# Kernel tuning notes

Measured on AMD Instinct MI355X. Metric: run time of the kernel, lower is better.

Reference implementation:

```python
import jax, jax.numpy as jnp
import numpy as np

B, S, A, H, Z = 256, 512, 64, 1024, 256

def setup_inputs() -> dict:
    key = jax.random.key(0)
    ks = jax.random.split(key, 24)
    w = lambda k, shape: (jax.random.normal(k, shape, jnp.float32) * 0.02)
    inp = {
        "x": jax.random.randint(ks[0], (B, S), 0, A),
        "h0": jax.random.normal(ks[1], (B, H), jnp.float32),            # init_hidden randn
        "eps": jax.random.normal(ks[2], (S + 1, B, Z), jnp.float32),     # reparam noise per step + final
        "phi_x_w": w(ks[3], (H, A)),  "phi_x_b": jnp.zeros((H,), jnp.float32),
        "enc_w1": w(ks[4], (H, 2 * H)), "enc_b1": jnp.zeros((H,), jnp.float32),
        "enc_w2": w(ks[5], (Z, H)),     "enc_b2": jnp.zeros((Z,), jnp.float32),
        "pri_w1": w(ks[6], (H, H)),     "pri_b1": jnp.zeros((H,), jnp.float32),
        "pri_w2": w(ks[7], (Z, H)),     "pri_b2": jnp.zeros((Z,), jnp.float32),
        "phi_z_w": w(ks[8], (H, Z)),    "phi_z_b": jnp.zeros((H,), jnp.float32),
        "dec_w": w(ks[9], (H, 2 * H)),  "dec_b": jnp.zeros((H,), jnp.float32),
        "act_w": w(ks[10], (A, H)),     "act_b": jnp.zeros((A,), jnp.float32),
        "gru_wih": w(ks[11], (3 * H, 2 * H)), "gru_whh": w(ks[12], (3 * H, H)),
        "gru_bih": jnp.zeros((3 * H,), jnp.float32), "gru_bhh": jnp.zeros((3 * H,), jnp.float32),
    }
    return inp

def reference(x, h0, eps, phi_x_w, phi_x_b, enc_w1, enc_b1, enc_w2, enc_b2,
              pri_w1, pri_b1, pri_w2, pri_b2, phi_z_w, phi_z_b, dec_w, dec_b,
              act_w, act_b, gru_wih, gru_whh, gru_bih, gru_bhh):
    relu, sp = jax.nn.relu, jax.nn.softplus

    def gru_cell(xin, h):  # PyTorch GRU gate math
        gi = xin @ gru_wih.T + gru_bih
        gh = h @ gru_whh.T + gru_bhh
        ir, iz, inn = jnp.split(gi, 3, axis=-1)
        hr, hz, hn = jnp.split(gh, 3, axis=-1)
        r = jax.nn.sigmoid(ir + hr)
        zg = jax.nn.sigmoid(iz + hz)
        n = jnp.tanh(inn + r * hn)
        return (1.0 - zg) * n + zg * h

    def prior(h):
        p = relu(h @ pri_w1.T + pri_b1) @ pri_w2.T + pri_b2
        return p, sp(p)

    x_oh = jax.nn.one_hot(x, A, dtype=jnp.float32).transpose(1, 0, 2)  # [S,B,A]

    def step(carry, inp):
        h, kld = carry
        x_t, eps_t = inp
        px = relu(x_t @ phi_x_w.T + phi_x_b)                            # [B,H]
        enc = relu(jnp.concatenate([px, h], -1) @ enc_w1.T + enc_b1) @ enc_w2.T + enc_b2
        enc_std = sp(enc)
        pri_m, pri_std = prior(h)
        kld_el = (2 * jnp.log(pri_std) - 2 * jnp.log(enc_std)
                  + (enc_std ** 2 + (enc - pri_m) ** 2) / pri_std ** 2 - 1.0)
        kld = kld + 0.5 * jnp.sum(kld_el)
        z_t = eps_t * enc_std + enc                                     # reparam sample
        pz = relu(z_t @ phi_z_w.T + phi_z_b)
        h_new = gru_cell(jnp.concatenate([px, pz], -1), h)
        return (h_new, kld), None

    (h, kld), _ = jax.lax.scan(step, (h0, jnp.float32(0.0)), (x_oh, eps[:S]))

    pri_m, pri_std = prior(h)
    z_t = eps[S] * pri_std + pri_m
    pz = relu(z_t @ phi_z_w.T + phi_z_b)
    dec = relu(jnp.concatenate([pz, h], -1) @ dec_w.T + dec_b)
    pred_act = dec @ act_w.T + act_b
    return pred_act, kld
```

## Files before the change

### kernel.cpp

```cpp
#include <hip/hip_runtime.h>


typedef float f32x4 __attribute__((ext_vector_type(4)));
typedef __bf16 bf16x8 __attribute__((ext_vector_type(8)));

#define BB 256
#define SS 512
#define HH 1024
#define ZZ 256
#define AA 64
#define NWG 256

__device__ __forceinline__ float softplus_(float x) {
    return (x > 15.f) ? x : log1pf(expf(x));
}
__device__ __forceinline__ float sigmoid_(float x) {
    return 1.f / (1.f + expf(-x));
}

__device__ __forceinline__ void gbar(unsigned* bar, unsigned p, int wg) {
    __syncthreads();
    if (threadIdx.x == 0) {
        unsigned s = p & 7u;
        unsigned exp = (p >> 3) + 1u;
        unsigned* leaf = bar + (s * 8 + (wg >> 5)) * 16;
        unsigned* root = bar + (64 + s) * 16;
        unsigned* flag = bar + (72 + s) * 16;
        unsigned old = __hip_atomic_fetch_add(leaf, 1u, __ATOMIC_ACQ_REL, __HIP_MEMORY_SCOPE_AGENT);
        if (old == 32u * exp - 1u) {
            unsigned old2 = __hip_atomic_fetch_add(root, 1u, __ATOMIC_ACQ_REL, __HIP_MEMORY_SCOPE_AGENT);
            if (old2 == 8u * exp - 1u) {
                __hip_atomic_store(flag, exp, __ATOMIC_RELEASE, __HIP_MEMORY_SCOPE_AGENT);
            }
        }
        while (__hip_atomic_load(flag, __ATOMIC_ACQUIRE, __HIP_MEMORY_SCOPE_AGENT) < exp) {
            __builtin_amdgcn_s_sleep(2);
        }
    }
    __syncthreads();
}

__device__ __forceinline__ void xbar(unsigned* flags, int g, int rank, int ngrp,
                                     unsigned tok) {
    __syncthreads();
    if (threadIdx.x == 0)
        __hip_atomic_store(flags + g * 256 + rank, tok, __ATOMIC_RELAXED,
                           __HIP_MEMORY_SCOPE_AGENT);
    unsigned l = threadIdx.x & 63;
    unsigned* base = flags + g * 256;
    for (;;) {
        bool ok = true;
        for (int i = (int)l; i < ngrp; i += 64)
            ok &= (__hip_atomic_load(base + i, __ATOMIC_RELAXED,
                                     __HIP_MEMORY_SCOPE_AGENT) >= tok);
        if (__all(ok)) break;
        __builtin_amdgcn_s_sleep(2);
    }
    asm volatile("buffer_inv sc0" ::: "memory");
}

template<int MT, int NT>
__device__ __forceinline__ void wgemm(const __bf16* __restrict__ A, int lda, int mstride,
                                      const __bf16* __restrict__ B, int ldb, int nstride,
                                      int K, f32x4 (&acc)[MT][NT]) {
    int lane = threadIdx.x & 63;
    int rr = lane & 15;
    int ko = (lane >> 4) * 8;
    const __bf16* ap = A + rr * lda + ko;
    const __bf16* bp = B + rr * ldb + ko;
    #pragma unroll 2
    for (int k = 0; k < K; k += 32) {
        bf16x8 af[MT], bfr[NT];
        #pragma unroll
        for (int mt = 0; mt < MT; mt++) af[mt] = *(const bf16x8*)(ap + mt * mstride + k);
        #pragma unroll
        for (int nt = 0; nt < NT; nt++) bfr[nt] = *(const bf16x8*)(bp + nt * nstride + k);
        #pragma unroll
        for (int mt = 0; mt < MT; mt++)
            #pragma unroll
            for (int nt = 0; nt < NT; nt++)
                acc[mt][nt] = __builtin_amdgcn_mfma_f32_16x16x32_bf16(af[mt], bfr[nt], acc[mt][nt], 0, 0, 0);
    }
}


__global__ void k_zeroctl(unsigned* bar, unsigned* flags, unsigned* cnt, float* kldacc) {
    for (int i = threadIdx.x; i < 1280; i += 256) bar[i] = 0u;
    for (int i = threadIdx.x; i < 2048; i += 256) flags[i] = 0u;
    if (threadIdx.x < 8) cnt[threadIdx.x] = 0u;
    if (threadIdx.x == 0) *kldacc = 0.f;
}

__global__ void k_pack(const float* __restrict__ src, int src_ld, int col_off,
                       __bf16* __restrict__ dst, int cols, int total) {
    int i = blockIdx.x * 256 + threadIdx.x;
    if (i >= total) return;
    int r = i / cols, c = i - r * cols;
    dst[i] = (__bf16)src[r * src_ld + col_off + c];
}

__global__ void k_copyf(const float* __restrict__ s, float* __restrict__ d, int n) {
    int i = blockIdx.x * 256 + threadIdx.x;
    if (i < n) d[i] = s[i];
}

__global__ void k_px(const float* __restrict__ phi_x_w, const float* __restrict__ phi_x_b,
                     float* __restrict__ px) {
    int i = blockIdx.x * 256 + threadIdx.x;
    int a = i >> 10, hh = i & 1023;
    px[i] = fmaxf(phi_x_w[hh * AA + a] + phi_x_b[hh], 0.f);
}

__global__ __launch_bounds__(256) void k_tables(const float* __restrict__ enc_w1,
                                                const float* __restrict__ wih,
                                                const float* __restrict__ px,
                                                float* __restrict__ encpx,
                                                float* __restrict__ gipx) {
    __shared__ float spx[64][65];
    int tid = threadIdx.x;
    int cg = blockIdx.x * 4 + (tid >> 6);
    int a = tid & 63;
    const float* wrow = (cg < 1024) ? (enc_w1 + cg * 2048) : (wih + (cg - 1024) * 2048);
    float sum = 0.f;
    for (int k0 = 0; k0 < 1024; k0 += 64) {
        __syncthreads();
        for (int e = tid; e < 4096; e += 256)
            spx[e >> 6][e & 63] = px[((e >> 6) << 10) + k0 + (e & 63)];
        __syncthreads();
        #pragma unroll 8
        for (int kk = 0; kk < 64; kk++) sum += wrow[k0 + kk] * spx[a][kk];
    }
    if (cg < 1024) encpx[a * 1024 + cg] = sum;
    else gipx[a * 3072 + (cg - 1024)] = sum;
}


struct PArgs {
    const int* x; const float* eps;
    const __bf16 *WA, *W2, *WPZ, *WIH, *WHH, *WDEC, *WACT;
    const float *encpx, *gipx;
    const float *eb1, *pb1, *eb2, *pb2, *pzb, *decb, *actb, *bih, *bhh;
    float *hf0, *hf1; __bf16 *hb0, *hb1;
    __bf16 *hidcat, *zbuf, *pzbuf, *tailhid, *decbuf;
    float *gh; float *kldacc; unsigned *bar, *flags, *cnt;
    float* out;
};

__global__ __launch_bounds__(256) void k_persist(PArgs a) {
    int wg = blockIdx.x;
    int tid = threadIdx.x;
    int v = tid >> 6;
    int lane = tid & 63;
    int rr = lane & 15;
    int ko = (lane >> 4) * 8;
    int col = lane & 15, rq = (lane >> 4) * 4;
    float kl = 0.f;
    float* hf[2] = {a.hf0, a.hf1};
    __bf16* hb[2] = {a.hb0, a.hb1};

    __shared__ float lds2[4][2][256];
    __shared__ int sh_g, sh_rank, sh_ngrp;
    __shared__ float sh_kl[4];

    if (tid == 0) {
        unsigned xcc = __builtin_amdgcn_s_getreg((31 << 11) | (0 << 6) | 20) & 7u;
        sh_g = (int)xcc;
        sh_rank = (int)atomicAdd(a.cnt + xcc, 1u);
    }
    __syncthreads();
    int g = sh_g, rank = sh_rank;
    gbar(a.bar, 0, wg);
    if (tid == 0)
        sh_ngrp = (int)__hip_atomic_load(a.cnt + g, __ATOMIC_RELAXED,
                                         __HIP_MEMORY_SCOPE_AGENT);
    __syncthreads();
    int ngrp = sh_ngrp;
    int base_m = g * 32;

    unsigned tok = 1;

    for (int t = 0; t < SS; t++) {
        int cur = t & 1, nxt = cur ^ 1;

        for (int r = rank; r < 32; r += ngrp) {
            int mt = v >> 1;
            int nt0 = r * 10 + (v & 1) * 5;
            const __bf16* ap = hb[cur] + (size_t)(base_m + mt * 16 + rr) * HH + ko;
            const __bf16* bp[5];
            #pragma unroll
            for (int j = 0; j < 5; j++) {
                int n = (nt0 + j) * 16 + rr;
                bp[j] = ((n < 2048) ? (a.WA + (size_t)n * HH)
                                    : (a.WHH + (size_t)(n - 2048) * HH)) + ko;
            }
            f32x4 acc[5] = {};
            #pragma unroll 2
            for (int k = 0; k < HH; k += 32) {
                bf16x8 af = *(const bf16x8*)(ap + k);
                #pragma unroll
                for (int j = 0; j < 5; j++)
                    acc[j] = __builtin_amdgcn_mfma_f32_16x16x32_bf16(
                        af, *(const bf16x8*)(bp[j] + k), acc[j], 0, 0, 0);
            }
            int xb[4];
            #pragma unroll
            for (int i = 0; i < 4; i++)
                xb[i] = a.x[(base_m + mt * 16 + rq + i) * SS + t];
            #pragma unroll
            for (int j = 0; j < 5; j++) {
                int c0 = (nt0 + j) * 16 + col;
                if (c0 < 1024) {
                    float bias = a.eb1[c0];
                    #pragma unroll
                    for (int i = 0; i < 4; i++) {
                        int m = base_m + mt * 16 + rq + i;
                        float val = acc[j][i] + bias + a.encpx[xb[i] * 1024 + c0];
                        a.hidcat[m * 2048 + c0] = (__bf16)fmaxf(val, 0.f);
                    }
                } else if (c0 < 2048) {
                    float bias = a.pb1[c0 - 1024];
                    #pragma unroll
                    for (int i = 0; i < 4; i++) {
                        int m = base_m + mt * 16 + rq + i;
                        a.hidcat[m * 2048 + c0] = (__bf16)fmaxf(acc[j][i] + bias, 0.f);
                    }
                } else {
                    int gc = c0 - 2048;
                    #pragma unroll
                    for (int i = 0; i < 4; i++) {
                        int m = base_m + mt * 16 + rq + i;
                        a.gh[m * 3072 + gc] = acc[j][i];
                    }
                }
            }
        }
        xbar(a.flags, g, rank, ngrp, tok++);

        for (int r = rank; r < 32; r += ngrp) {
            int mtl = r >> 4, zsl = r & 15;
            const __bf16* ae_p = a.hidcat + (size_t)(base_m + mtl * 16 + rr) * 2048 + v * 256 + ko;
            const __bf16* ap_p = ae_p + 1024;
            const __bf16* be_p = a.W2 + (size_t)(zsl * 16 + rr) * HH + v * 256 + ko;
            const __bf16* bp_p = a.W2 + (size_t)(256 + zsl * 16 + rr) * HH + v * 256 + ko;
            f32x4 ae = {0.f,0.f,0.f,0.f}, av = {0.f,0.f,0.f,0.f};
            #pragma unroll
            for (int k = 0; k < 256; k += 32) {
                ae = __builtin_amdgcn_mfma_f32_16x16x32_bf16(
                    *(const bf16x8*)(ae_p + k), *(const bf16x8*)(be_p + k), ae, 0, 0, 0);
                av = __builtin_amdgcn_mfma_f32_16x16x32_bf16(
                    *(const bf16x8*)(ap_p + k), *(const bf16x8*)(bp_p + k), av, 0, 0, 0);
            }
            #pragma unroll
            for (int i = 0; i < 4; i++) {
                int idx = (rq + i) * 16 + col;
                lds2[v][0][idx] = ae[i];
                lds2[v][1][idx] = av[i];
            }
            __syncthreads();
            {
                float e = lds2[0][0][tid] + lds2[1][0][tid] + lds2[2][0][tid] + lds2[3][0][tid];
                float pv = lds2[0][1][tid] + lds2[1][1][tid] + lds2[2][1][tid] + lds2[3][1][tid];
                int m = base_m + mtl * 16 + (tid >> 4);
                int z = zsl * 16 + (tid & 15);
                float enc = e + a.eb2[z];
                float pri = pv + a.pb2[z];
                float es = softplus_(enc), ps = softplus_(pri);
                float d = enc - pri;
                kl += 2.f * (logf(ps) - logf(es)) + (es * es + d * d) / (ps * ps) - 1.f;
                const float* epst = a.eps + (size_t)t * BB * ZZ;
                a.zbuf[m * ZZ + z] = (__bf16)(epst[m * ZZ + z] * es + enc);
            }
            __syncthreads();
        }
        xbar(a.flags, g, rank, ngrp, tok++);

        for (int r = rank; r < 32; r += ngrp) {
            int mt = v >> 1;
            int nt = r * 2 + (v & 1);
            const __bf16* ap = a.zbuf + (size_t)(base_m + mt * 16 + rr) * ZZ + ko;
            const __bf16* bp = a.WPZ + (size_t)(nt * 16 + rr) * ZZ + ko;
            f32x4 acc = {0.f,0.f,0.f,0.f};
            #pragma unroll
            for (int k = 0; k < ZZ; k += 32)
                acc = __builtin_amdgcn_mfma_f32_16x16x32_bf16(
                    *(const bf16x8*)(ap + k), *(const bf16x8*)(bp + k), acc, 0, 0, 0);
            int n = nt * 16 + col;
            float b = a.pzb[n];
            #pragma unroll
            for (int i = 0; i < 4; i++) {
                int m = base_m + mt * 16 + rq + i;
                a.pzbuf[m * HH + n] = (__bf16)fmaxf(acc[i] + b, 0.f);
            }
        }
        xbar(a.flags, g, rank, ngrp, tok++);

        for (int r = rank; r < 32; r += ngrp) {
            int mt = v >> 1;
            int jt = r * 2 + (v & 1);
            const __bf16* ap = a.pzbuf + (size_t)(base_m + mt * 16 + rr) * HH + ko;
            const __bf16* bp0 = a.WIH + (size_t)(jt * 16 + rr) * HH + ko;
            const __bf16* bp1g = bp0 + (size_t)1024 * HH;
            const __bf16* bp2g = bp0 + (size_t)2048 * HH;
            f32x4 acc[3] = {};
            #pragma unroll 2
            for (int k = 0; k < HH; k += 32) {
                bf16x8 af = *(const bf16x8*)(ap + k);
                acc[0] = __builtin_amdgcn_mfma_f32_16x16x32_bf16(af, *(const bf16x8*)(bp0 + k), acc[0], 0, 0, 0);
                acc[1] = __builtin_amdgcn_mfma_f32_16x16x32_bf16(af, *(const bf16x8*)(bp1g + k), acc[1], 0, 0, 0);
                acc[2] = __builtin_amdgcn_mfma_f32_16x16x32_bf16(af, *(const bf16x8*)(bp2g + k), acc[2], 0, 0, 0);
            }
            int j = jt * 16 + col;
            float br = a.bih[j], bz2 = a.bih[1024 + j], bn = a.bih[2048 + j];
            float cr = a.bhh[j], cz = a.bhh[1024 + j], cn = a.bhh[2048 + j];
            #pragma unroll
            for (int i = 0; i < 4; i++) {
                int m = base_m + mt * 16 + rq + i;
                int xb = a.x[m * SS + t];
                const float* gp = a.gipx + xb * 3072;
                float gir = acc[0][i] + gp[j] + br;
                float giz = acc[1][i] + gp[1024 + j] + bz2;
                float gin = acc[2][i] + gp[2048 + j] + bn;
                float ghr = a.gh[m * 3072 + j] + cr;
                float ghz = a.gh[m * 3072 + 1024 + j] + cz;
                float ghn = a.gh[m * 3072 + 2048 + j] + cn;
                float rg = sigmoid_(gir + ghr);
                float zg = sigmoid_(giz + ghz);
                float nn = tanhf(gin + rg * ghn);
                float hv = (1.f - zg) * nn + zg * hf[cur][m * HH + j];
                hf[nxt][m * HH + j] = hv;
                hb[nxt][m * HH + j] = (__bf16)hv;
            }
        }
        xbar(a.flags, g, rank, ngrp, tok++);
    }

    for (int r = rank; r < 32; r += ngrp) {
        int mt = v >> 1, nt = r * 2 + (v & 1);
        f32x4 acc[1][1] = {};
        wgemm<1, 1>(hb[0] + (size_t)(base_m + mt * 16) * HH, HH, 0,
                    a.WA + (size_t)(1024 + nt * 16) * HH, HH, 0, HH, acc);
        int n = nt * 16 + col;
        float b = a.pb1[n];
        #pragma unroll
        for (int i = 0; i < 4; i++) {
            int m = base_m + mt * 16 + rq + i;
            a.tailhid[m * HH + n] = (__bf16)fmaxf(acc[0][0][i] + b, 0.f);
        }
    }
    xbar(a.flags, g, rank, ngrp, tok++);
    if (v == 0) {
        for (int r = rank; r < 32; r += ngrp) {
            int mtl = r >> 4, zt = r & 15;
            f32x4 apv[1][1] = {};
            wgemm<1, 1>(a.tailhid + (size_t)(base_m + mtl * 16) * HH, HH, 0,
                        a.W2 + (size_t)(256 + zt * 16) * HH, HH, 0, HH, apv);
            int z = zt * 16 + col;
            float bp = a.pb2[z];
            const float* epst = a.eps + (size_t)SS * BB * ZZ;
            #pragma unroll
            for (int i = 0; i < 4; i++) {
                int m = base_m + mtl * 16 + rq + i;
                float pri = apv[0][0][i] + bp;
                float ps = softplus_(pri);
                a.zbuf[m * ZZ + z] = (__bf16)(epst[m * ZZ + z] * ps + pri);
            }
        }
    }
    xbar(a.flags, g, rank, ngrp, tok++);
    for (int r = rank; r < 32; r += ngrp) {
        int mt = v >> 1, nt = r * 2 + (v & 1);
        f32x4 acc[1][1] = {};
        wgemm<1, 1>(a.zbuf + (size_t)(base_m + mt * 16) * ZZ, ZZ, 0,
                    a.WPZ + (size_t)(nt * 16) * ZZ, ZZ, 0, ZZ, acc);
        int n = nt * 16 + col;
        float b = a.pzb[n];
        #pragma unroll
        for (int i = 0; i < 4; i++) {
            int m = base_m + mt * 16 + rq + i;
            a.pzbuf[m * HH + n] = (__bf16)fmaxf(acc[0][0][i] + b, 0.f);
        }
    }
    xbar(a.flags, g, rank, ngrp, tok++);
    for (int r = rank; r < 32; r += ngrp) {
        int mt = v >> 1, nt = r * 2 + (v & 1);
        f32x4 acc[1][1] = {};
        wgemm<1, 1>(a.pzbuf + (size_t)(base_m + mt * 16) * HH, HH, 0,
                    a.WDEC + (size_t)(nt * 16) * 2048, 2048, 0, HH, acc);
        wgemm<1, 1>(hb[0] + (size_t)(base_m + mt * 16) * HH, HH, 0,
                    a.WDEC + (size_t)(nt * 16) * 2048 + 1024, 2048, 0, HH, acc);
        int n = nt * 16 + col;
        float b = a.decb[n];
        #pragma unroll
        for (int i = 0; i < 4; i++) {
            int m = base_m + mt * 16 + rq + i;
            a.decbuf[m * HH + n] = (__bf16)fmaxf(acc[0][0][i] + b, 0.f);
        }
    }
    xbar(a.flags, g, rank, ngrp, tok++);
    if (v == 0) {
        for (int r = rank; r < 32; r += ngrp) {
            if (r >= 8) continue;
            int mt = r >> 2, nt = r & 3;
            f32x4 acc[1][1] = {};
            wgemm<1, 1>(a.decbuf + (size_t)(base_m + mt * 16) * HH, HH, 0,
                        a.WACT + (size_t)(nt * 16) * HH, HH, 0, HH, acc);
            int n = nt * 16 + col;
            float b = a.actb[n];
            #pragma unroll
            for (int i = 0; i < 4; i++) {
                int m = base_m + mt * 16 + rq + i;
                a.out[m * AA + n] = acc[0][0][i] + b;
            }
        }
    }

    {
        float s = kl;
        #pragma unroll
        for (int off = 1; off < 64; off <<= 1) s += __shfl_xor(s, off);
        if (lane == 0) sh_kl[v] = s;
        __syncthreads();
        if (tid == 0) {
            float ws = sh_kl[0] + sh_kl[1] + sh_kl[2] + sh_kl[3];
            atomicAdd(a.kldacc, ws);
        }
    }
    gbar(a.bar, 1, wg);
    if (wg == 0 && tid == 0) {
        float s = __hip_atomic_load(a.kldacc, __ATOMIC_ACQUIRE, __HIP_MEMORY_SCOPE_AGENT);
        a.out[BB * AA] = 0.5f * s;
    }
}

extern "C" void kernel_launch(void* const* d_in, const int* in_sizes, int n_in,
                              void* d_out, int out_size, void* d_ws, size_t ws_size,
                              hipStream_t stream) {
    const int*   x       = (const int*)d_in[0];
    const float* h0      = (const float*)d_in[1];
    const float* eps     = (const float*)d_in[2];
    const float* phi_x_w = (const float*)d_in[3];
    const float* phi_x_b = (const float*)d_in[4];
    const float* enc_w1  = (const float*)d_in[5];
    const float* enc_b1  = (const float*)d_in[6];
    const float* enc_w2  = (const float*)d_in[7];
    const float* enc_b2  = (const float*)d_in[8];
    const float* pri_w1  = (const float*)d_in[9];
    const float* pri_b1  = (const float*)d_in[10];
    const float* pri_w2  = (const float*)d_in[11];
    const float* pri_b2  = (const float*)d_in[12];
    const float* phi_z_w = (const float*)d_in[13];
    const float* phi_z_b = (const float*)d_in[14];
    const float* dec_w   = (const float*)d_in[15];
    const float* dec_b   = (const float*)d_in[16];
    const float* act_w   = (const float*)d_in[17];
    const float* act_b   = (const float*)d_in[18];
    const float* gru_wih = (const float*)d_in[19];
    const float* gru_whh = (const float*)d_in[20];
    const float* gru_bih = (const float*)d_in[21];
    const float* gru_bhh = (const float*)d_in[22];

    char* p = (char*)d_ws;
    auto alloc = [&](size_t bytes) { char* r = p; p += (bytes + 255) & ~(size_t)255; return r; };

    __bf16* WA    = (__bf16*)alloc(2048 * 1024 * 2);
    __bf16* W2    = (__bf16*)alloc(512 * 1024 * 2);
    __bf16* WPZ   = (__bf16*)alloc(1024 * 256 * 2);
    __bf16* WIH   = (__bf16*)alloc(3072 * 1024 * 2);
    __bf16* WHH   = (__bf16*)alloc(3072 * 1024 * 2);
    __bf16* WDEC  = (__bf16*)alloc(1024 * 2048 * 2);
    __bf16* WACT  = (__bf16*)alloc(64 * 1024 * 2);
    float*  px    = (float*)alloc(64 * 1024 * 4);
    float*  encpx = (float*)alloc(64 * 1024 * 4);
    float*  gipx  = (float*)alloc(64 * 3072 * 4);
    float*  hf0   = (float*)alloc(BB * HH * 4);
    float*  hf1   = (float*)alloc(BB * HH * 4);
    __bf16* hb0   = (__bf16*)alloc(BB * HH * 2);
    __bf16* hb1   = (__bf16*)alloc(BB * HH * 2);
    __bf16* hidcat = (__bf16*)alloc(BB * 2048 * 2);
    __bf16* zbuf   = (__bf16*)alloc(BB * ZZ * 2);
    __bf16* pzbuf  = (__bf16*)alloc(BB * HH * 2);
    __bf16* tailhid = (__bf16*)alloc(BB * HH * 2);
    __bf16* decbuf  = (__bf16*)alloc(BB * HH * 2);
    float*  gh     = (float*)alloc(BB * 3072 * 4);
    unsigned* bar  = (unsigned*)alloc(1280 * 4);
    unsigned* flags = (unsigned*)alloc(2048 * 4);
    unsigned* cnt  = (unsigned*)alloc(64 * 4);
    float*  kldacc = (float*)alloc(256);

    auto pack = [&](const float* src, int src_ld, int off, __bf16* dst, int rows, int cols) {
        int total = rows * cols;
        k_pack<<<(total + 255) / 256, 256, 0, stream>>>(src, src_ld, off, dst, cols, total);
    };

    k_zeroctl<<<1, 256, 0, stream>>>(bar, flags, cnt, kldacc);
    pack(enc_w1, 2048, 1024, WA, 1024, 1024);
    pack(pri_w1, 1024, 0, WA + 1024 * 1024, 1024, 1024);
    pack(enc_w2, 1024, 0, W2, 256, 1024);
    pack(pri_w2, 1024, 0, W2 + 256 * 1024, 256, 1024);
    pack(phi_z_w, 256, 0, WPZ, 1024, 256);
    pack(gru_wih, 2048, 1024, WIH, 3072, 1024);
    pack(gru_whh, 1024, 0, WHH, 3072, 1024);
    pack(dec_w, 2048, 0, WDEC, 1024, 2048);
    pack(act_w, 1024, 0, WACT, 64, 1024);
    pack(h0, 1024, 0, hb0, 256, 1024);
    k_copyf<<<(BB * HH + 255) / 256, 256, 0, stream>>>(h0, hf0, BB * HH);
    k_px<<<(64 * 1024) / 256, 256, 0, stream>>>(phi_x_w, phi_x_b, px);
    k_tables<<<1024, 256, 0, stream>>>(enc_w1, gru_wih, px, encpx, gipx);

    PArgs pa;
    pa.x = x; pa.eps = eps;
    pa.WA = WA; pa.W2 = W2; pa.WPZ = WPZ; pa.WIH = WIH; pa.WHH = WHH;
    pa.WDEC = WDEC; pa.WACT = WACT;
    pa.encpx = encpx; pa.gipx = gipx;
    pa.eb1 = enc_b1; pa.pb1 = pri_b1; pa.eb2 = enc_b2; pa.pb2 = pri_b2;
    pa.pzb = phi_z_b; pa.decb = dec_b; pa.actb = act_b;
    pa.bih = gru_bih; pa.bhh = gru_bhh;
    pa.hf0 = hf0; pa.hf1 = hf1; pa.hb0 = hb0; pa.hb1 = hb1;
    pa.hidcat = hidcat; pa.zbuf = zbuf; pa.pzbuf = pzbuf;
    pa.tailhid = tailhid; pa.decbuf = decbuf;
    pa.gh = gh; pa.kldacc = kldacc;
    pa.bar = bar; pa.flags = flags; pa.cnt = cnt;
    pa.out = (float*)d_out;

    k_persist<<<dim3(NWG), dim3(256), 0, stream>>>(pa);
}
```

Baseline: 29.21 ms.

## Double block size to 8 waves with split-K GEMMs and LDS reduction

Launches the persistent kernel with 512 threads per block instead of 256. The per-step hidden GEMM and the GRU input GEMM now split K across two wave halves, exchanging partial accumulators through a padded LDS buffer. The encoder/prior reduction stage spreads K over 8 waves, and the smaller stages are restricted to the first 4 waves. The goal is more waves in flight per CU to hide memory latency on the serial recurrence, at the cost of extra __syncthreads, LDS traffic and higher register pressure under launch_bounds(512,1).

```diff
diff --git a/kernel.cpp b/kernel.cpp
--- a/kernel.cpp
+++ b/kernel.cpp
@@ -10,6 +10,7 @@
 #define ZZ 256
 #define AA 64
 #define NWG 256
+#define MFMA __builtin_amdgcn_mfma_f32_16x16x32_bf16
 
 __device__ __forceinline__ float softplus_(float x) {
     return (x > 15.f) ? x : log1pf(expf(x));
@@ -79,7 +80,7 @@
         for (int mt = 0; mt < MT; mt++)
             #pragma unroll
             for (int nt = 0; nt < NT; nt++)
-                acc[mt][nt] = __builtin_amdgcn_mfma_f32_16x16x32_bf16(af[mt], bfr[nt], acc[mt][nt], 0, 0, 0);
+                acc[mt][nt] = MFMA(af[mt], bfr[nt], acc[mt][nt], 0, 0, 0);
     }
 }
 
@@ -146,7 +147,7 @@
     float* out;
 };
 
-__global__ __launch_bounds__(256) void k_persist(PArgs a) {
+__global__ __launch_bounds__(512, 1) void k_persist(PArgs a) {
     int wg = blockIdx.x;
     int tid = threadIdx.x;
     int v = tid >> 6;
@@ -158,9 +159,10 @@
     float* hf[2] = {a.hf0, a.hf1};
     __bf16* hb[2] = {a.hb0, a.hb1};
 
-    __shared__ float lds2[4][2][256];
+    __shared__ float ldsC[5440];
+    __shared__ float lds2[8][2][272];
     __shared__ int sh_g, sh_rank, sh_ngrp;
-    __shared__ float sh_kl[4];
+    __shared__ float sh_kl[8];
 
     if (tid == 0) {
         unsigned xcc = __builtin_amdgcn_s_getreg((31 << 11) | (0 << 6) | 20) & 7u;
@@ -183,83 +185,99 @@
         int cur = t & 1, nxt = cur ^ 1;
 
         for (int r = rank; r < 32; r += ngrp) {
-            int mt = v >> 1;
-            int nt0 = r * 10 + (v & 1) * 5;
-            const __bf16* ap = hb[cur] + (size_t)(base_m + mt * 16 + rr) * HH + ko;
+            int mt = v & 1, nh = (v >> 1) & 1, kh = v >> 2;
+            int nt0 = r * 10 + nh * 5;
+            const __bf16* ap = hb[cur] + (size_t)(base_m + mt * 16 + rr) * HH + kh * 512 + ko;
             const __bf16* bp[5];
             #pragma unroll
             for (int j = 0; j < 5; j++) {
                 int n = (nt0 + j) * 16 + rr;
                 bp[j] = ((n < 2048) ? (a.WA + (size_t)n * HH)
-                                    : (a.WHH + (size_t)(n - 2048) * HH)) + ko;
+                                    : (a.WHH + (size_t)(n - 2048) * HH)) + kh * 512 + ko;
             }
             f32x4 acc[5] = {};
-            #pragma unroll 2
-            for (int k = 0; k < HH; k += 32) {
+            #pragma unroll 4
+            for (int k = 0; k < 512; k += 32) {
                 bf16x8 af = *(const bf16x8*)(ap + k);
                 #pragma unroll
                 for (int j = 0; j < 5; j++)
-                    acc[j] = __builtin_amdgcn_mfma_f32_16x16x32_bf16(
-                        af, *(const bf16x8*)(bp[j] + k), acc[j], 0, 0, 0);
-            }
-            int xb[4];
-            #pragma unroll
-            for (int i = 0; i < 4; i++)
-                xb[i] = a.x[(base_m + mt * 16 + rq + i) * SS + t];
+                    acc[j] = MFMA(af, *(const bf16x8*)(bp[j] + k), acc[j], 0, 0, 0);
+            }
+            int iw = (kh ^ 1) * 2;
+            #pragma unroll
+            for (int j = 0; j < 5; j++)
+                #pragma unroll
+                for (int d = 0; d < 2; d++)
+                    ldsC[((mt * 2 + nh) * 5 + j) * 272 + (rq + iw + d) * 17 + col] = acc[j][iw + d];
+            __syncthreads();
+            int ir = kh * 2;
+            int xb[2];
+            #pragma unroll
+            for (int d = 0; d < 2; d++)
+                xb[d] = a.x[(base_m + mt * 16 + rq + ir + d) * SS + t];
             #pragma unroll
             for (int j = 0; j < 5; j++) {
                 int c0 = (nt0 + j) * 16 + col;
+                float fin[2];
+                #pragma unroll
+                for (int d = 0; d < 2; d++)
+                    fin[d] = acc[j][ir + d] +
+                             ldsC[((mt * 2 + nh) * 5 + j) * 272 + (rq + ir + d) * 17 + col];
                 if (c0 < 1024) {
                     float bias = a.eb1[c0];
                     #pragma unroll
-                    for (int i = 0; i < 4; i++) {
-                        int m = base_m + mt * 16 + rq + i;
-                        float val = acc[j][i] + bias + a.encpx[xb[i] * 1024 + c0];
+                    for (int d = 0; d < 2; d++) {
+                        int m = base_m + mt * 16 + rq + ir + d;
+                        float val = fin[d] + bias + a.encpx[xb[d] * 1024 + c0];
                         a.hidcat[m * 2048 + c0] = (__bf16)fmaxf(val, 0.f);
                     }
                 } else if (c0 < 2048) {
                     float bias = a.pb1[c0 - 1024];
                     #pragma unroll
-                    for (int i = 0; i < 4; i++) {
-                        int m = base_m + mt * 16 + rq + i;
-                        a.hidcat[m * 2048 + c0] = (__bf16)fmaxf(acc[j][i] + bias, 0.f);
+                    for (int d = 0; d < 2; d++) {
+                        int m = base_m + mt * 16 + rq + ir + d;
+                        a.hidcat[m * 2048 + c0] = (__bf16)fmaxf(fin[d] + bias, 0.f);
                     }
                 } else {
                     int gc = c0 - 2048;
                     #pragma unroll
-                    for (int i = 0; i < 4; i++) {
-                        int m = base_m + mt * 16 + rq + i;
-                        a.gh[m * 3072 + gc] = acc[j][i];
+                    for (int d = 0; d < 2; d++) {
+                        int m = base_m + mt * 16 + rq + ir + d;
+                        a.gh[m * 3072 + gc] = fin[d];
                     }
                 }
             }
+            __syncthreads();
         }
         xbar(a.flags, g, rank, ngrp, tok++);
 
         for (int r = rank; r < 32; r += ngrp) {
             int mtl = r >> 4, zsl = r & 15;
-            const __bf16* ae_p = a.hidcat + (size_t)(base_m + mtl * 16 + rr) * 2048 + v * 256 + ko;
+            const __bf16* ae_p = a.hidcat + (size_t)(base_m + mtl * 16 + rr) * 2048 + v * 128 + ko;
             const __bf16* ap_p = ae_p + 1024;
-            const __bf16* be_p = a.W2 + (size_t)(zsl * 16 + rr) * HH + v * 256 + ko;
-            const __bf16* bp_p = a.W2 + (size_t)(256 + zsl * 16 + rr) * HH + v * 256 + ko;
+            const __bf16* be_p = a.W2 + (size_t)(zsl * 16 + rr) * HH + v * 128 + ko;
+            const __bf16* bp_p = a.W2 + (size_t)(256 + zsl * 16 + rr) * HH + v * 128 + ko;
             f32x4 ae = {0.f,0.f,0.f,0.f}, av = {0.f,0.f,0.f,0.f};
             #pragma unroll
-            for (int k = 0; k < 256; k += 32) {
-                ae = __builtin_amdgcn_mfma_f32_16x16x32_bf16(
-                    *(const bf16x8*)(ae_p + k), *(const bf16x8*)(be_p + k), ae, 0, 0, 0);
-                av = __builtin_amdgcn_mfma_f32_16x16x32_bf16(
-                    *(const bf16x8*)(ap_p + k), *(const bf16x8*)(bp_p + k), av, 0, 0, 0);
+            for (int k = 0; k < 128; k += 32) {
+                ae = MFMA(*(const bf16x8*)(ae_p + k), *(const bf16x8*)(be_p + k), ae, 0, 0, 0);
+                av = MFMA(*(const bf16x8*)(ap_p + k), *(const bf16x8*)(bp_p + k), av, 0, 0, 0);
             }
             #pragma unroll
             for (int i = 0; i < 4; i++) {
-                int idx = (rq + i) * 16 + col;
+                int idx = (rq + i) * 17 + col;
                 lds2[v][0][idx] = ae[i];
                 lds2[v][1][idx] = av[i];
             }
             __syncthreads();
-            {
-                float e = lds2[0][0][tid] + lds2[1][0][tid] + lds2[2][0][tid] + lds2[3][0][tid];
-                float pv = lds2[0][1][tid] + lds2[1][1][tid] + lds2[2][1][tid] + lds2[3][1][tid];
+            if (tid < 256) {
+                int idx = (tid >> 4) * 17 + (tid & 15);
+                float e = 0.f, pv = 0.f;
+                #pragma unroll
+                for (int w8 = 0; w8 < 8; w8++) {
+                    e += lds2[w8][0][idx];
+                    pv += lds2[w8][1][idx];
+                }
                 int m = base_m + mtl * 16 + (tid >> 4);
                 int z = zsl * 16 + (tid & 15);
                 float enc = e + a.eb2[z];
@@ -274,52 +292,66 @@
         }
         xbar(a.flags, g, rank, ngrp, tok++);
 
-        for (int r = rank; r < 32; r += ngrp) {
-            int mt = v >> 1;
-            int nt = r * 2 + (v & 1);
-            const __bf16* ap = a.zbuf + (size_t)(base_m + mt * 16 + rr) * ZZ + ko;
-            const __bf16* bp = a.WPZ + (size_t)(nt * 16 + rr) * ZZ + ko;
-            f32x4 acc = {0.f,0.f,0.f,0.f};
-            #pragma unroll
-            for (int k = 0; k < ZZ; k += 32)
-                acc = __builtin_amdgcn_mfma_f32_16x16x32_bf16(
-                    *(const bf16x8*)(ap + k), *(const bf16x8*)(bp + k), acc, 0, 0, 0);
-            int n = nt * 16 + col;
-            float b = a.pzb[n];
-            #pragma unroll
-            for (int i = 0; i < 4; i++) {
-                int m = base_m + mt * 16 + rq + i;
-                a.pzbuf[m * HH + n] = (__bf16)fmaxf(acc[i] + b, 0.f);
+        if (v < 4) {
+            for (int r = rank; r < 32; r += ngrp) {
+                int mt = v >> 1;
+                int nt = r * 2 + (v & 1);
+                const __bf16* ap = a.zbuf + (size_t)(base_m + mt * 16 + rr) * ZZ + ko;
+                const __bf16* bp = a.WPZ + (size_t)(nt * 16 + rr) * ZZ + ko;
+                f32x4 acc = {0.f,0.f,0.f,0.f};
+                #pragma unroll
+                for (int k = 0; k < ZZ; k += 32)
+                    acc = MFMA(*(const bf16x8*)(ap + k), *(const bf16x8*)(bp + k), acc, 0, 0, 0);
+                int n = nt * 16 + col;
+                float b = a.pzb[n];
+                #pragma unroll
+                for (int i = 0; i < 4; i++) {
+                    int m = base_m + mt * 16 + rq + i;
+                    a.pzbuf[m * HH + n] = (__bf16)fmaxf(acc[i] + b, 0.f);
+                }
             }
         }
         xbar(a.flags, g, rank, ngrp, tok++);
 
         for (int r = rank; r < 32; r += ngrp) {
-            int mt = v >> 1;
-            int jt = r * 2 + (v & 1);
-            const __bf16* ap = a.pzbuf + (size_t)(base_m + mt * 16 + rr) * HH + ko;
-            const __bf16* bp0 = a.WIH + (size_t)(jt * 16 + rr) * HH + ko;
+            int mt = v & 1, jh = (v >> 1) & 1, kh = v >> 2;
+            int jt = r * 2 + jh;
+            const __bf16* ap = a.pzbuf + (size_t)(base_m + mt * 16 + rr) * HH + kh * 512 + ko;
+            const __bf16* bp0 = a.WIH + (size_t)(jt * 16 + rr) * HH + kh * 512 + ko;
             const __bf16* bp1g = bp0 + (size_t)1024 * HH;
             const __bf16* bp2g = bp0 + (size_t)2048 * HH;
             f32x4 acc[3] = {};
-            #pragma unroll 2
-            for (int k = 0; k < HH; k += 32) {
+            #pragma unroll 4
+            for (int k = 0; k < 512; k += 32) {
                 bf16x8 af = *(const bf16x8*)(ap + k);
-                acc[0] = __builtin_amdgcn_mfma_f32_16x16x32_bf16(af, *(const bf16x8*)(bp0 + k), acc[0], 0, 0, 0);
-                acc[1] = __builtin_amdgcn_mfma_f32_16x16x32_bf16(af, *(const bf16x8*)(bp1g + k), acc[1], 0, 0, 0);
-                acc[2] = __builtin_amdgcn_mfma_f32_16x16x32_bf16(af, *(const bf16x8*)(bp2g + k), acc[2], 0, 0, 0);
-            }
+                acc[0] = MFMA(af, *(const bf16x8*)(bp0 + k), acc[0], 0, 0, 0);
+                acc[1] = MFMA(af, *(const bf16x8*)(bp1g + k), acc[1], 0, 0, 0);
+                acc[2] = MFMA(af, *(const bf16x8*)(bp2g + k), acc[2], 0, 0, 0);
+            }
+            int iw = (kh ^ 1) * 2;
+            #pragma unroll
+            for (int g3 = 0; g3 < 3; g3++)
+                #pragma unroll
+                for (int d = 0; d < 2; d++)
+                    ldsC[((mt * 2 + jh) * 3 + g3) * 272 + (rq + iw + d) * 17 + col] = acc[g3][iw + d];
+            __syncthreads();
+            int ir = kh * 2;
             int j = jt * 16 + col;
             float br = a.bih[j], bz2 = a.bih[1024 + j], bn = a.bih[2048 + j];
             float cr = a.bhh[j], cz = a.bhh[1024 + j], cn = a.bhh[2048 + j];
             #pragma unroll
-            for (int i = 0; i < 4; i++) {
-                int m = base_m + mt * 16 + rq + i;
+            for (int d = 0; d < 2; d++) {
+                float fin[3];
+                #pragma unroll
+                for (int g3 = 0; g3 < 3; g3++)
+                    fin[g3] = acc[g3][ir + d] +
+                              ldsC[((mt * 2 + jh) * 3 + g3) * 272 + (rq + ir + d) * 17 + col];
+                int m = base_m + mt * 16 + rq + ir + d;
                 int xb = a.x[m * SS + t];
-                const float* gp = a.gipx + xb * 3072;
-                float gir = acc[0][i] + gp[j] + br;
-                float giz = acc[1][i] + gp[1024 + j] + bz2;
-                float gin = acc[2][i] + gp[2048 + j] + bn;
+                const float* gp = a.gipx + (size_t)xb * 3072;
+                float gir = fin[0] + gp[j] + br;
+                float giz = fin[1] + gp[1024 + j] + bz2;
+                float gin = fin[2] + gp[2048 + j] + bn;
                 float ghr = a.gh[m * 3072 + j] + cr;
                 float ghz = a.gh[m * 3072 + 1024 + j] + cz;
                 float ghn = a.gh[m * 3072 + 2048 + j] + cn;
@@ -330,21 +362,24 @@
                 hf[nxt][m * HH + j] = hv;
                 hb[nxt][m * HH + j] = (__bf16)hv;
             }
+            __syncthreads();
         }
         xbar(a.flags, g, rank, ngrp, tok++);
     }
 
-    for (int r = rank; r < 32; r += ngrp) {
-        int mt = v >> 1, nt = r * 2 + (v & 1);
-        f32x4 acc[1][1] = {};
-        wgemm<1, 1>(hb[0] + (size_t)(base_m + mt * 16) * HH, HH, 0,
-                    a.WA + (size_t)(1024 + nt * 16) * HH, HH, 0, HH, acc);
-        int n = nt * 16 + col;
-        float b = a.pb1[n];
-        #pragma unroll
-        for (int i = 0; i < 4; i++) {
-            int m = base_m + mt * 16 + rq + i;
-            a.tailhid[m * HH + n] = (__bf16)fmaxf(acc[0][0][i] + b, 0.f);
+    if (v < 4) {
+        for (int r = rank; r < 32; r += ngrp) {
+            int mt = v >> 1, nt = r * 2 + (v & 1);
+            f32x4 acc[1][1] = {};
+            wgemm<1, 1>(hb[0] + (size_t)(base_m + mt * 16) * HH, HH, 0,
+                        a.WA + (size_t)(1024 + nt * 16) * HH, HH, 0, HH, acc);
+            int n = nt * 16 + col;
+            float b = a.pb1[n];
+            #pragma unroll
+            for (int i = 0; i < 4; i++) {
+                int m = base_m + mt * 16 + rq + i;
+                a.tailhid[m * HH + n] = (__bf16)fmaxf(acc[0][0][i] + b, 0.f);
+            }
         }
     }
     xbar(a.flags, g, rank, ngrp, tok++);
@@ -367,33 +402,37 @@
         }
     }
     xbar(a.flags, g, rank, ngrp, tok++);
-    for (int r = rank; r < 32; r += ngrp) {
-        int mt = v >> 1, nt = r * 2 + (v & 1);
-        f32x4 acc[1][1] = {};
-        wgemm<1, 1>(a.zbuf + (size_t)(base_m + mt * 16) * ZZ, ZZ, 0,
-                    a.WPZ + (size_t)(nt * 16) * ZZ, ZZ, 0, ZZ, acc);
-        int n = nt * 16 + col;
-        float b = a.pzb[n];
-        #pragma unroll
-        for (int i = 0; i < 4; i++) {
-            int m = base_m + mt * 16 + rq + i;
-            a.pzbuf[m * HH + n] = (__bf16)fmaxf(acc[0][0][i] + b, 0.f);
+    if (v < 4) {
+        for (int r = rank; r < 32; r += ngrp) {
+            int mt = v >> 1, nt = r * 2 + (v & 1);
+            f32x4 acc[1][1] = {};
+            wgemm<1, 1>(a.zbuf + (size_t)(base_m + mt * 16) * ZZ, ZZ, 0,
+                        a.WPZ + (size_t)(nt * 16) * ZZ, ZZ, 0, ZZ, acc);
+            int n = nt * 16 + col;
+            float b = a.pzb[n];
+            #pragma unroll
+            for (int i = 0; i < 4; i++) {
+                int m = base_m + mt * 16 + rq + i;
+                a.pzbuf[m * HH + n] = (__bf16)fmaxf(acc[0][0][i] + b, 0.f);
+            }
         }
     }
     xbar(a.flags, g, rank, ngrp, tok++);
-    for (int r = rank; r < 32; r += ngrp) {
-        int mt = v >> 1, nt = r * 2 + (v & 1);
-        f32x4 acc[1][1] = {};
-        wgemm<1, 1>(a.pzbuf + (size_t)(base_m + mt * 16) * HH, HH, 0,
-                    a.WDEC + (size_t)(nt * 16) * 2048, 2048, 0, HH, acc);
-        wgemm<1, 1>(hb[0] + (size_t)(base_m + mt * 16) * HH, HH, 0,
-                    a.WDEC + (size_t)(nt * 16) * 2048 + 1024, 2048, 0, HH, acc);
-        int n = nt * 16 + col;
-        float b = a.decb[n];
-        #pragma unroll
-        for (int i = 0; i < 4; i++) {
-            int m = base_m + mt * 16 + rq + i;
-            a.decbuf[m * HH + n] = (__bf16)fmaxf(acc[0][0][i] + b, 0.f);
+    if (v < 4) {
+        for (int r = rank; r < 32; r += ngrp) {
+            int mt = v >> 1, nt = r * 2 + (v & 1);
+            f32x4 acc[1][1] = {};
+            wgemm<1, 1>(a.pzbuf + (size_t)(base_m + mt * 16) * HH, HH, 0,
+                        a.WDEC + (size_t)(nt * 16) * 2048, 2048, 0, HH, acc);
+            wgemm<1, 1>(hb[0] + (size_t)(base_m + mt * 16) * HH, HH, 0,
+                        a.WDEC + (size_t)(nt * 16) * 2048 + 1024, 2048, 0, HH, acc);
+            int n = nt * 16 + col;
+            float b = a.decb[n];
+            #pragma unroll
+            for (int i = 0; i < 4; i++) {
+                int m = base_m + mt * 16 + rq + i;
+                a.decbuf[m * HH + n] = (__bf16)fmaxf(acc[0][0][i] + b, 0.f);
+            }
         }
     }
     xbar(a.flags, g, rank, ngrp, tok++);
@@ -421,7 +460,9 @@
         if (lane == 0) sh_kl[v] = s;
         __syncthreads();
         if (tid == 0) {
-            float ws = sh_kl[0] + sh_kl[1] + sh_kl[2] + sh_kl[3];
+            float ws = 0.f;
+            #pragma unroll
+            for (int w8 = 0; w8 < 8; w8++) ws += sh_kl[w8];
             atomicAdd(a.kldacc, ws);
         }
     }
@@ -522,5 +563,5 @@
     pa.bar = bar; pa.flags = flags; pa.cnt = cnt;
     pa.out = (float*)d_out;
 
-    k_persist<<<dim3(NWG), dim3(256), 0, stream>>>(pa);
-}
+    k_persist<<<dim3(NWG), dim3(512), 0, stream>>>(pa);
+}
```

After: 29.06 ms. Within noise of the previous version (-0.5%).
